# Kernel tuning notes

Hardware: AMD Instinct MI355X
Metric: run time of the kernel (lower is better)

## Reference

```python
import jax, jax.numpy as jnp
import numpy as np

DIM = 128      # input node feature dim
GS = 64        # SAGEConv output dim
AF = 32        # additional (ir_score) feature dim
NB = 2         # nb_classes
G = 8192       # num_graphs in batch
NPG = 16       # nodes per graph
N = G * NPG    # total nodes = 131072
E = 2097152    # total edges (avg degree 16)


def setup_inputs() -> dict:
    key = jax.random.key(0)
    ks = jax.random.split(key, 10)

    def w(k, shape, fan_in):
        return jax.random.normal(k, shape, jnp.float32) / np.sqrt(fan_in)

    return {
        "x": jax.random.normal(ks[0], (N, DIM), jnp.float32),
        "edge_index": jax.random.randint(ks[1], (2, E), 0, N),
        "set_indices": jax.random.randint(ks[2], (G, 2), 0, NPG),
        "batch_ids": jnp.repeat(jnp.arange(G), NPG),  # sorted graph ids, PyG style
        "ir_score": jax.random.uniform(ks[3], (G, AF), jnp.float32),
        "W_l": w(ks[4], (DIM, GS), DIM),
        "b_l": jnp.zeros((GS,), jnp.float32),
        "W_r": w(ks[5], (DIM, GS), DIM),
        "W_ir": w(ks[6], (AF, 2 * GS), AF),
        "b_ir": jnp.zeros((2 * GS,), jnp.float32),
        "W1": w(ks[7], ((2 * GS) * (2 * GS), 200), (2 * GS) * (2 * GS)),
        "b1": jnp.zeros((200,), jnp.float32),
        "W2": w(ks[8], (200, NB), 200),
        "b2": jnp.zeros((NB,), jnp.float32),
    }


def reference(x, edge_index, set_indices, batch_ids, ir_score,
              W_l, b_l, W_r, W_ir, b_ir, W1, b1, W2, b2):
    n = x.shape[0]
    src, dst = edge_index[0], edge_index[1]

    # SAGEConv (mean aggregation): out = lin_l(mean_{j in N(i)} x_j) + lin_r(x_i)
    agg = jax.ops.segment_sum(x[src], dst, num_segments=n)           # [N, DIM]
    deg = jax.ops.segment_sum(jnp.ones((src.shape[0],), x.dtype), dst, num_segments=n)
    mean = agg / jnp.maximum(deg, 1.0)[:, None]
    h = jax.nn.relu(mean @ W_l + b_l + x @ W_r)                      # [N, GS]

    # per-graph node counts -> index bases (cumsum), then global pair indices
    g = set_indices.shape[0]
    num_nodes = jax.ops.segment_sum(jnp.ones((n,), jnp.float32), batch_ids, num_segments=g)
    csum = jnp.cumsum(num_nodes.astype(jnp.int64))
    index_bases = jnp.concatenate([jnp.zeros((1,), jnp.int64), csum[:-1]])
    sib = index_bases[:, None] + set_indices                         # [G, 2]

    pair = h[sib].reshape(g, 2 * GS)                                 # gather + flatten

    # fusion: relu(linear(ir_score)) then per-graph outer product
    S = jax.nn.relu(ir_score @ W_ir + b_ir)                          # [G, 2*GS]
    outer = jnp.einsum('gi,gj->gij', pair, S).reshape(g, -1)         # [G, (2GS)^2]

    # decode MLP
    z = jax.nn.relu(outer @ W1 + b1)                                 # [G, 200]
    logits = z @ W2 + b2                                             # [G, NB]
    return logits
```

## Files before the change

### kernel.cpp

```cpp
#include <hip/hip_runtime.h>

#define NN   131072
#define GG   8192
#define EE   2097152
#define KBIG 16384
#define NPAD 224
#define NSPLIT 8
#define NSEL  16384
#define SBUCK 1024
#define SUBC  4
#define SCAPS 112
#define SCAPT (SUBC*SCAPS)

typedef _Float16 half_t;
typedef __attribute__((ext_vector_type(8))) _Float16 half8;
typedef __attribute__((ext_vector_type(4))) _Float16 half4;
typedef __attribute__((ext_vector_type(4))) float floatx4;

__device__ inline floatx4 mfma16(half8 a, half8 b, floatx4 c) {
  return __builtin_amdgcn_mfma_f32_16x16x32_f16(a, b, c, 0, 0, 0);
}

__global__ __launch_bounds__(256) void prep_all(const float* __restrict__ Wl,
                                                const float* __restrict__ Wr,
                                                const float* __restrict__ W1,
                                                const int* __restrict__ setix,
                                                half_t* __restrict__ Wt,
                                                half_t* __restrict__ W1p,
                                                int* __restrict__ slot_node,
                                                int* __restrict__ scnt) {
  int b = blockIdx.x, tid = threadIdx.x;
  if (b < 1792) {
    int idx = b * 256 + tid;
    int lane = idx & 63;
    int t = idx >> 6;
    int nt = t % 14; t /= 14;
    int jj = t & 1;  t >>= 1;
    int i  = t & 15; t >>= 4;
    int ph = t & 1;  t >>= 1;
    int split = t;
    int n = nt * 16 + (lane & 15);
    int k0 = split * 2048 + i * 128 + ph * 64 + jj * 32 + (lane >> 4) * 8;
    half8 v;
#pragma unroll
    for (int e = 0; e < 8; e++)
      v[e] = (half_t)((n < 200) ? W1[(size_t)(k0 + e) * 200 + n] : 0.f);
    *(half8*)(W1p + (size_t)idx * 8) = v;
  } else if (b < 1856) {
    int idx = (b - 1792) * 256 + tid;
    int n = idx >> 7, k = idx & 127;
    float v = (n < 64) ? Wl[k * 64 + n] : Wr[k * 64 + (n - 64)];
    Wt[n * 128 + k] = (half_t)v;
  } else if (b < 1920) {
    int idx = (b - 1856) * 256 + tid;
    slot_node[idx] = (idx >> 1) * 16 + setix[idx];
  } else {
    int idx = (b - 1920) * 256 + tid;
    scnt[idx] = 0;
  }
}

__global__ __launch_bounds__(256) void fused_mid(const float* __restrict__ x,
                                                 const half_t* __restrict__ WtG,
                                                 const float* __restrict__ b_l,
                                                 const int* __restrict__ slot_node,
                                                 const int* __restrict__ setix,
                                                 const int* __restrict__ src,
                                                 const int* __restrict__ dst,
                                                 int* __restrict__ scnt,
                                                 unsigned int* __restrict__ sbuf,
                                                 half_t* __restrict__ y16,
                                                 half_t* __restrict__ r_slot) {
  __shared__ half_t wlds[64 * 128];
  __shared__ half_t ybuf[64 * 72];
  int b = blockIdx.x, tid = threadIdx.x;
  if (b < 2048) {
    int w = tid >> 6, lane = tid & 63;
    int m = lane & 15, q = lane >> 4, kc = q * 8;
#pragma unroll
    for (int it = 0; it < 4; it++) {
      int cb = (it * 4 + w) * 64;
      const half_t* g = WtG + ((size_t)cb + lane) * 8;
      half_t* l = wlds + (size_t)cb * 8;
      __builtin_amdgcn_global_load_lds((const __attribute__((address_space(1))) uint32_t*)g,
                                       (__attribute__((address_space(3))) uint32_t*)l, 16, 0, 0);
    }
    int node0 = b * 64 + w * 16;
    float4 xu[4][2];
#pragma unroll
    for (int step = 0; step < 4; step++) {
      const float* xp = x + (size_t)(node0 + m) * 128 + step * 32 + kc;
      xu[step][0] = *(const float4*)xp;
      xu[step][1] = *(const float4*)(xp + 4);
    }
    __syncthreads();
    floatx4 acc[4];
#pragma unroll
    for (int nt = 0; nt < 4; nt++) acc[nt] = (floatx4){0.f, 0.f, 0.f, 0.f};
#pragma unroll
    for (int step = 0; step < 4; step++) {
      float4 u0 = xu[step][0], u1 = xu[step][1];
      half8 av = {(half_t)u0.x, (half_t)u0.y, (half_t)u0.z, (half_t)u0.w,
                  (half_t)u1.x, (half_t)u1.y, (half_t)u1.z, (half_t)u1.w};
      int k0 = step * 32 + kc;
#pragma unroll
      for (int nt = 0; nt < 4; nt++) {
        half8 bv = *(const half8*)(wlds + (nt * 16 + m) * 128 + k0);
        acc[nt] = mfma16(av, bv, acc[nt]);
      }
    }
#pragma unroll
    for (int nt = 0; nt < 4; nt++)
#pragma unroll
      for (int r = 0; r < 4; r++)
        ybuf[(w * 16 + q * 4 + r) * 72 + nt * 16 + m] = (half_t)acc[nt][r];
    asm volatile("s_waitcnt lgkmcnt(0)" ::: "memory");
    __builtin_amdgcn_sched_barrier(0);
#pragma unroll
    for (int it = 0; it < 2; it++) {
      int ch = lane + it * 64;
      int row = ch >> 3, co = (ch & 7) * 8;
      *(half8*)(y16 + (size_t)(node0 + row) * 64 + co) =
          *(const half8*)(ybuf + (w * 16 + row) * 72 + co);
    }
  } else if (b < 2304) {
    int w = tid >> 6, lane = tid & 63;
    int m = lane & 15, q = lane >> 4, kc = q * 8;
    int s0 = (b - 2048) * 64 + w * 16;
    int node = slot_node[s0 + m];
    floatx4 acc[4];
#pragma unroll
    for (int nt = 0; nt < 4; nt++) acc[nt] = (floatx4){0.f, 0.f, 0.f, 0.f};
#pragma unroll
    for (int step = 0; step < 4; step++) {
      int k0 = step * 32 + kc;
      const float* xp = x + (size_t)node * 128 + k0;
      float4 u0 = *(const float4*)xp;
      float4 u1 = *(const float4*)(xp + 4);
      half8 av = {(half_t)u0.x, (half_t)u0.y, (half_t)u0.z, (half_t)u0.w,
                  (half_t)u1.x, (half_t)u1.y, (half_t)u1.z, (half_t)u1.w};
#pragma unroll
      for (int nt = 0; nt < 4; nt++) {
        half8 bv = *(const half8*)(WtG + (size_t)(64 + nt * 16 + m) * 128 + k0);
        acc[nt] = mfma16(av, bv, acc[nt]);
      }
    }
#pragma unroll
    for (int nt = 0; nt < 4; nt++) {
      int n = nt * 16 + m;
      float bias = b_l[n];
#pragma unroll
      for (int r = 0; r < 4; r++) {
        int s = s0 + q * 4 + r;
        r_slot[(size_t)s * 64 + n] = (half_t)(acc[nt][r] + bias);
      }
    }
  } else {
    int eb = b - 2304;
    int e = eb * 256 + tid;
    int d = dst[e];
    int g = d >> 4, local = d & 15;
    int si0 = setix[g * 2], si1 = setix[g * 2 + 1];
    int slot = (local == si0) ? g * 2 : ((local == si1) ? g * 2 + 1 : -1);
    if (slot >= 0) {
      int bk = slot >> 4;
      int sub = eb & (SUBC - 1);
      int pos = atomicAdd(&scnt[(bk * SUBC + sub) * 16], 1);
      if (pos < SCAPS)
        sbuf[(size_t)(bk * SUBC + sub) * SCAPS + pos] =
            (unsigned int)src[e] | ((unsigned int)(slot & 15) << 17);
    }
  }
}

__global__ __launch_bounds__(256) void slot_agg(const unsigned int* __restrict__ sbuf,
                                                const int* __restrict__ scnt,
                                                const half_t* __restrict__ y16,
                                                const half_t* __restrict__ r_slot,
                                                half_t* __restrict__ h_slot) {
  __shared__ int sorted[SCAPT];
  __shared__ int hist[16];
  __shared__ int base[16];
  __shared__ int start[17];
  int b = blockIdx.x, tid = threadIdx.x;
  if (tid < 16) hist[tid] = 0;
  __syncthreads();
  unsigned int myedge[SUBC];
  int mycnt = 0;
#pragma unroll
  for (int sub = 0; sub < SUBC; sub++) {
    int n = scnt[(b * SUBC + sub) * 16]; if (n > SCAPS) n = SCAPS;
    const unsigned int* eb = sbuf + (size_t)(b * SUBC + sub) * SCAPS;
    for (int e = tid; e < n; e += 256) {
      unsigned int pk = eb[e];
      myedge[mycnt++] = pk;
      atomicAdd(&hist[pk >> 17], 1);
    }
  }
  __syncthreads();
  if (tid < 16) {
    int v = hist[tid];
    int sum = v;
#pragma unroll
    for (int off = 1; off < 16; off <<= 1) {
      int u = __shfl_up(sum, off);
      if (tid >= off) sum += u;
    }
    start[tid] = sum - v;
    base[tid]  = sum - v;
    if (tid == 15) start[16] = sum;
  }
  __syncthreads();
  for (int i = 0; i < mycnt; i++) {
    unsigned int pk = myedge[i];
    int pos = atomicAdd(&base[pk >> 17], 1);
    sorted[pos] = (int)(pk & 0x1FFFF);
  }
  __syncthreads();
  int s = tid >> 4, p = tid & 15;
  int e0 = start[s], e1 = start[s + 1];
  float a0 = 0.f, a1 = 0.f, a2 = 0.f, a3 = 0.f;
  int e = e0;
  for (; e + 2 <= e1; e += 2) {
    int n0 = sorted[e], n1 = sorted[e + 1];
    half4 v0 = *(const half4*)(y16 + (size_t)n0 * 64 + p * 4);
    half4 v1 = *(const half4*)(y16 + (size_t)n1 * 64 + p * 4);
    a0 += (float)v0[0] + (float)v1[0];
    a1 += (float)v0[1] + (float)v1[1];
    a2 += (float)v0[2] + (float)v1[2];
    a3 += (float)v0[3] + (float)v1[3];
  }
  if (e < e1) {
    int n0 = sorted[e];
    half4 v0 = *(const half4*)(y16 + (size_t)n0 * 64 + p * 4);
    a0 += (float)v0[0]; a1 += (float)v0[1]; a2 += (float)v0[2]; a3 += (float)v0[3];
  }
  int slot = b * 16 + s;
  float inv = 1.0f / fmaxf((float)(e1 - e0), 1.0f);
  half4 rr = *(const half4*)(r_slot + (size_t)slot * 64 + p * 4);
  half4 o;
  o[0] = (half_t)fmaxf(a0 * inv + (float)rr[0], 0.f);
  o[1] = (half_t)fmaxf(a1 * inv + (float)rr[1], 0.f);
  o[2] = (half_t)fmaxf(a2 * inv + (float)rr[2], 0.f);
  o[3] = (half_t)fmaxf(a3 * inv + (float)rr[3], 0.f);
  *(half4*)(h_slot + (size_t)slot * 64 + p * 4) = o;
}

__global__ void s_pair_kernel(const float* __restrict__ ir, const float* __restrict__ W_ir,
                              const float* __restrict__ b_ir, half_t* __restrict__ S16,
                              const half_t* __restrict__ h_slot,
                              const int* __restrict__ set_idx, half_t* __restrict__ pair16) {
  int idx = blockIdx.x * blockDim.x + threadIdx.x;
  int g = idx >> 7, o = idx & 127;
  const float* irow = ir + g * 32;
  float sv = b_ir[o];
#pragma unroll
  for (int a = 0; a < 32; a++) sv += irow[a] * W_ir[a * 128 + o];
  S16[idx] = (half_t)fmaxf(sv, 0.f);
  int which = o >> 6, c = o & 63;
  int li = set_idx[g * 2 + which];
  int slot = (li == set_idx[g * 2]) ? g * 2 : g * 2 + 1;
  pair16[idx] = h_slot[(size_t)slot * 64 + c];
}

__global__ __launch_bounds__(256, 2) void biggemm(const half_t* __restrict__ pair16,
                                                  const half_t* __restrict__ S16,
                                                  const half_t* __restrict__ W1p,
                                                  float* __restrict__ zpart) {
  __shared__ __align__(16) half_t bbuf[2][28 * 512];
  __shared__ half_t pls[16][128];
  int bx = blockIdx.x;
  int mt = bx >> 3, split = bx & 7;
  int g0 = mt * 128;
  int tid = threadIdx.x, w = tid >> 6, lane = tid & 63;
  int wm = w >> 1, wn = w & 1;
  int m = lane & 15, q = lane >> 4, kc = q * 8;
  int ntb = wn * 7;

  auto stage = [&](int ph, int ii, int buf) {
#pragma unroll
    for (int ff = 0; ff < 7; ff++) {
      int f = ff * 4 + w;
      const half_t* gsrc = W1p + ((((size_t)(split * 2 + ph) * 16 + ii) * 28) + f) * 512 + lane * 8;
      half_t* ldst = &bbuf[buf][f * 512];
      __builtin_amdgcn_global_load_lds((const __attribute__((address_space(1))) uint32_t*)gsrc,
                                       (__attribute__((address_space(3))) uint32_t*)ldst, 16, 0, 0);
    }
  };

  stage(0, 0, 0);

  {
    int row = tid & 127, sel = tid >> 7;
    half8 pa = *(const half8*)(pair16 + (size_t)(g0 + row) * 128 + split * 16 + sel * 8);
#pragma unroll
    for (int j = 0; j < 8; j++) pls[sel * 8 + j][row] = pa[j];
  }

  floatx4 acc[4][7];
#pragma unroll
  for (int sb = 0; sb < 4; sb++)
#pragma unroll
    for (int t = 0; t < 7; t++) acc[sb][t] = (floatx4){0.f, 0.f, 0.f, 0.f};

  half8 sf[4][2];
#pragma unroll
  for (int ph = 0; ph < 2; ph++) {
#pragma unroll
    for (int sub = 0; sub < 4; sub++) {
      int grow = g0 + wm * 64 + sub * 16 + m;
#pragma unroll
      for (int j2 = 0; j2 < 2; j2++)
        sf[sub][j2] = *(const half8*)(S16 + (size_t)grow * 128 + ph * 64 + j2 * 32 + kc);
    }
#pragma unroll
    for (int i = 0; i < 16; i++) {
      int s = ph * 16 + i;
      int cur = s & 1;
      __syncthreads();
      half_t p0 = pls[i][wm * 64 + 0 * 16 + m];
      half_t p1 = pls[i][wm * 64 + 1 * 16 + m];
      half_t p2 = pls[i][wm * 64 + 2 * 16 + m];
      half_t p3 = pls[i][wm * 64 + 3 * 16 + m];
      if (s < 31) {
        int s1 = s + 1;
        stage(s1 >> 4, s1 & 15, cur ^ 1);
      }
      const half_t* bb = bbuf[cur];
#pragma unroll
      for (int jj = 0; jj < 2; jj++) {
        half8 a0 = sf[0][jj] * p0;
        half8 a1 = sf[1][jj] * p1;
        half8 a2 = sf[2][jj] * p2;
        half8 a3 = sf[3][jj] * p3;
#pragma unroll
        for (int t = 0; t < 7; t++) {
          half8 bv = *(const half8*)(bb + (jj * 14 + ntb + t) * 512 + lane * 8);
          acc[0][t] = mfma16(a0, bv, acc[0][t]);
          acc[1][t] = mfma16(a1, bv, acc[1][t]);
          acc[2][t] = mfma16(a2, bv, acc[2][t]);
          acc[3][t] = mfma16(a3, bv, acc[3][t]);
        }
      }
    }
  }

#pragma unroll
  for (int sub = 0; sub < 4; sub++)
#pragma unroll
    for (int t = 0; t < 7; t++)
#pragma unroll
      for (int r = 0; r < 4; r++) {
        int row = g0 + wm * 64 + sub * 16 + q * 4 + r;
        zpart[((size_t)split * GG + row) * NPAD + (ntb + t) * 16 + m] = acc[sub][t][r];
      }
}

__global__ __launch_bounds__(256) void reduce_mlp(const float* __restrict__ zpart,
                                                  const float* __restrict__ b1,
                                                  const float* __restrict__ W2,
                                                  const float* __restrict__ b2,
                                                  float* __restrict__ out) {
  int tid = threadIdx.x;
  int w = tid >> 6, lane = tid & 63;
  int g = blockIdx.x * 4 + w;
  float p0 = 0.f, p1 = 0.f;
#pragma unroll
  for (int qq = 0; qq < 4; qq++) {
    int c = qq * 64 + lane;
    if (c < 200) {
      float z = 0.f;
#pragma unroll
      for (int sp = 0; sp < NSPLIT; sp++)
        z += zpart[((size_t)sp * GG + g) * NPAD + c];
      z += b1[c];
      z = fmaxf(z, 0.f);
      p0 += z * W2[c * 2];
      p1 += z * W2[c * 2 + 1];
    }
  }
#pragma unroll
  for (int off = 32; off; off >>= 1) {
    p0 += __shfl_down(p0, off);
    p1 += __shfl_down(p1, off);
  }
  if (lane == 0) {
    out[g * 2] = p0 + b2[0];
    out[g * 2 + 1] = p1 + b2[1];
  }
}

extern "C" void kernel_launch(void* const* d_in, const int* in_sizes, int n_in,
                              void* d_out, int out_size, void* d_ws, size_t ws_size,
                              hipStream_t stream) {
  const float* x     = (const float*)d_in[0];
  const int*   ei    = (const int*)d_in[1];
  const int*   setix = (const int*)d_in[2];
  const float* ir    = (const float*)d_in[4];
  const float* W_l   = (const float*)d_in[5];
  const float* b_l   = (const float*)d_in[6];
  const float* W_r   = (const float*)d_in[7];
  const float* W_ir  = (const float*)d_in[8];
  const float* b_ir  = (const float*)d_in[9];
  const float* W1    = (const float*)d_in[10];
  const float* b1    = (const float*)d_in[11];
  const float* W2    = (const float*)d_in[12];
  const float* b2    = (const float*)d_in[13];
  float* out = (float*)d_out;

  char* ws = (char*)d_ws;
  size_t off = 0;
  auto alloc = [&](size_t bytes) -> void* {
    void* p = ws + off;
    off = (off + bytes + 255) & ~(size_t)255;
    return p;
  };
  size_t pool_start = off;
  int* slot_node = (int*)alloc((size_t)NSEL * 4);
  int* scnt      = (int*)alloc((size_t)SBUCK * SUBC * 16 * 4);
  unsigned int* sbuf = (unsigned int*)alloc((size_t)SBUCK * SUBC * SCAPS * 4);
  half_t* y16    = (half_t*)alloc((size_t)NN * 64 * 2);
  half_t* r_slot = (half_t*)alloc((size_t)NSEL * 64 * 2);
  half_t* h_slot = (half_t*)alloc((size_t)NSEL * 64 * 2);
  float* zpart = (float*)(ws + pool_start);
  {
    size_t zend = pool_start + (((size_t)NSPLIT * GG * NPAD * 4 + 255) & ~(size_t)255);
    if (off < zend) off = zend;
  }
  half_t* Wt     = (half_t*)alloc(128 * 128 * 2);
  half_t* W1p    = (half_t*)alloc((size_t)NPAD * KBIG * 2);
  half_t* S16    = (half_t*)alloc((size_t)GG * 128 * 2);
  half_t* pair16 = (half_t*)alloc((size_t)GG * 128 * 2);
  (void)ws_size; (void)in_sizes; (void)n_in; (void)out_size;

  const int* esrc = ei;
  const int* edst = ei + EE;

  prep_all<<<2176, 256, 0, stream>>>(W_l, W_r, W1, setix, Wt, W1p, slot_node, scnt);
  fused_mid<<<10496, 256, 0, stream>>>(x, Wt, b_l, slot_node, setix, esrc, edst,
                                       scnt, sbuf, y16, r_slot);
  slot_agg<<<SBUCK, 256, 0, stream>>>(sbuf, scnt, y16, r_slot, h_slot);
  s_pair_kernel<<<(GG * 128) / 256, 256, 0, stream>>>(ir, W_ir, b_ir, S16, h_slot, setix, pair16);
  biggemm<<<(GG / 128) * NSPLIT, 256, 0, stream>>>(pair16, S16, W1p, zpart);
  reduce_mlp<<<GG / 4, 256, 0, stream>>>(zpart, b1, W2, b2, out);
}
```

Measured before the change: 254.8 us.

## Fold S computation into prep and pair scatter into slot_agg; drop s_pair kernel

Moves the ir_score linear+relu into extra blocks of the prep kernel and has slot_agg write directly into the pair buffer, handling duplicate set indices by writing both halves, so the separate s_pair kernel and h_slot buffer go away. The edge-scan blocks in fused_mid now each process two edges per thread using an int2 load of dst, which halves that part of the grid. This removes one kernel launch and an intermediate round trip through global memory, at the cost of more work per thread in the edge scan.

Result: no change. 252.3 us (-1.0%).

```diff
diff --git a/kernel.cpp b/kernel.cpp
--- a/kernel.cpp
+++ b/kernel.cpp
@@ -25,10 +25,14 @@
                                                 const float* __restrict__ Wr,
                                                 const float* __restrict__ W1,
                                                 const int* __restrict__ setix,
+                                                const float* __restrict__ ir,
+                                                const float* __restrict__ W_ir,
+                                                const float* __restrict__ b_ir,
                                                 half_t* __restrict__ Wt,
                                                 half_t* __restrict__ W1p,
                                                 int* __restrict__ slot_node,
-                                                int* __restrict__ scnt) {
+                                                int* __restrict__ scnt,
+                                                half_t* __restrict__ S16) {
   int b = blockIdx.x, tid = threadIdx.x;
   if (b < 1792) {
     int idx = b * 256 + tid;
@@ -54,9 +58,17 @@
   } else if (b < 1920) {
     int idx = (b - 1856) * 256 + tid;
     slot_node[idx] = (idx >> 1) * 16 + setix[idx];
-  } else {
+  } else if (b < 2176) {
     int idx = (b - 1920) * 256 + tid;
     scnt[idx] = 0;
+  } else {
+    int idx = (b - 2176) * 256 + tid;
+    int g = idx >> 7, o = idx & 127;
+    const float* irow = ir + g * 32;
+    float sv = b_ir[o];
+#pragma unroll
+    for (int a = 0; a < 32; a++) sv += irow[a] * W_ir[a * 128 + o];
+    S16[idx] = (half_t)fmaxf(sv, 0.f);
   }
 }
 
@@ -157,18 +169,22 @@
     }
   } else {
     int eb = b - 2304;
-    int e = eb * 256 + tid;
-    int d = dst[e];
-    int g = d >> 4, local = d & 15;
-    int si0 = setix[g * 2], si1 = setix[g * 2 + 1];
-    int slot = (local == si0) ? g * 2 : ((local == si1) ? g * 2 + 1 : -1);
-    if (slot >= 0) {
-      int bk = slot >> 4;
-      int sub = eb & (SUBC - 1);
-      int pos = atomicAdd(&scnt[(bk * SUBC + sub) * 16], 1);
-      if (pos < SCAPS)
-        sbuf[(size_t)(bk * SUBC + sub) * SCAPS + pos] =
-            (unsigned int)src[e] | ((unsigned int)(slot & 15) << 17);
+    int e = (eb * 256 + tid) * 2;
+    int2 d2 = *(const int2*)(dst + e);
+#pragma unroll
+    for (int u = 0; u < 2; u++) {
+      int d = (u == 0) ? d2.x : d2.y;
+      int g = d >> 4, local = d & 15;
+      int si0 = setix[g * 2], si1 = setix[g * 2 + 1];
+      int slot = (local == si0) ? g * 2 : ((local == si1) ? g * 2 + 1 : -1);
+      if (slot >= 0) {
+        int bk = slot >> 4;
+        int sub = eb & (SUBC - 1);
+        int pos = atomicAdd(&scnt[(bk * SUBC + sub) * 16], 1);
+        if (pos < SCAPS)
+          sbuf[(size_t)(bk * SUBC + sub) * SCAPS + pos] =
+              (unsigned int)src[e + u] | ((unsigned int)(slot & 15) << 17);
+      }
     }
   }
 }
@@ -177,7 +193,8 @@
                                                 const int* __restrict__ scnt,
                                                 const half_t* __restrict__ y16,
                                                 const half_t* __restrict__ r_slot,
-                                                half_t* __restrict__ h_slot) {
+                                                const int* __restrict__ setix,
+                                                half_t* __restrict__ pair16) {
   __shared__ int sorted[SCAPT];
   __shared__ int hist[16];
   __shared__ int base[16];
@@ -243,24 +260,11 @@
   o[1] = (half_t)fmaxf(a1 * inv + (float)rr[1], 0.f);
   o[2] = (half_t)fmaxf(a2 * inv + (float)rr[2], 0.f);
   o[3] = (half_t)fmaxf(a3 * inv + (float)rr[3], 0.f);
-  *(half4*)(h_slot + (size_t)slot * 64 + p * 4) = o;
-}
-
-__global__ void s_pair_kernel(const float* __restrict__ ir, const float* __restrict__ W_ir,
-                              const float* __restrict__ b_ir, half_t* __restrict__ S16,
-                              const half_t* __restrict__ h_slot,
-                              const int* __restrict__ set_idx, half_t* __restrict__ pair16) {
-  int idx = blockIdx.x * blockDim.x + threadIdx.x;
-  int g = idx >> 7, o = idx & 127;
-  const float* irow = ir + g * 32;
-  float sv = b_ir[o];
-#pragma unroll
-  for (int a = 0; a < 32; a++) sv += irow[a] * W_ir[a * 128 + o];
-  S16[idx] = (half_t)fmaxf(sv, 0.f);
-  int which = o >> 6, c = o & 63;
-  int li = set_idx[g * 2 + which];
-  int slot = (li == set_idx[g * 2]) ? g * 2 : g * 2 + 1;
-  pair16[idx] = h_slot[(size_t)slot * 64 + c];
+  int g = slot >> 1, which = slot & 1;
+  bool dup = (setix[g * 2] == setix[g * 2 + 1]);
+  half_t* pr = pair16 + (size_t)g * 128 + which * 64 + p * 4;
+  if (!(which == 1 && dup)) *(half4*)pr = o;
+  if (which == 0 && dup)    *(half4*)(pr + 64) = o;
 }
 
 __global__ __launch_bounds__(256, 2) void biggemm(const half_t* __restrict__ pair16,
@@ -421,7 +425,6 @@
   unsigned int* sbuf = (unsigned int*)alloc((size_t)SBUCK * SUBC * SCAPS * 4);
   half_t* y16    = (half_t*)alloc((size_t)NN * 64 * 2);
   half_t* r_slot = (half_t*)alloc((size_t)NSEL * 64 * 2);
-  half_t* h_slot = (half_t*)alloc((size_t)NSEL * 64 * 2);
   float* zpart = (float*)(ws + pool_start);
   {
     size_t zend = pool_start + (((size_t)NSPLIT * GG * NPAD * 4 + 255) & ~(size_t)255);
@@ -436,11 +439,11 @@
   const int* esrc = ei;
   const int* edst = ei + EE;
 
-  prep_all<<<2176, 256, 0, stream>>>(W_l, W_r, W1, setix, Wt, W1p, slot_node, scnt);
-  fused_mid<<<10496, 256, 0, stream>>>(x, Wt, b_l, slot_node, setix, esrc, edst,
-                                       scnt, sbuf, y16, r_slot);
-  slot_agg<<<SBUCK, 256, 0, stream>>>(sbuf, scnt, y16, r_slot, h_slot);
-  s_pair_kernel<<<(GG * 128) / 256, 256, 0, stream>>>(ir, W_ir, b_ir, S16, h_slot, setix, pair16);
+  prep_all<<<6272, 256, 0, stream>>>(W_l, W_r, W1, setix, ir, W_ir, b_ir,
+                                     Wt, W1p, slot_node, scnt, S16);
+  fused_mid<<<6400, 256, 0, stream>>>(x, Wt, b_l, slot_node, setix, esrc, edst,
+                                      scnt, sbuf, y16, r_slot);
+  slot_agg<<<SBUCK, 256, 0, stream>>>(sbuf, scnt, y16, r_slot, setix, pair16);
   biggemm<<<(GG / 128) * NSPLIT, 256, 0, stream>>>(pair16, S16, W1p, zpart);
   reduce_mlp<<<GG / 4, 256, 0, stream>>>(zpart, b1, W2, b2, out);
 }
```
